# Kernel tuning notes

Hardware: AMD Instinct MI355X
Metric: run time of the kernel (lower is better)

Reference implementation:

```python
import jax, jax.numpy as jnp
import numpy as np

N = 16384      # nodes per graph (128x128 image)
E = 9 * N      # 8-neighborhood + self edges
C = 512        # input feature channels
M = 32         # matrixSize


def _p(key, shape, scale=0.05):
    return jax.random.normal(key, shape, dtype=jnp.float32) * scale


def setup_inputs() -> dict:
    key = jax.random.key(0)
    ks = jax.random.split(key, 40)
    inp = {
        "cF": jax.random.normal(ks[0], (N, C), dtype=jnp.float32),
        "sF": jax.random.normal(ks[1], (N, C), dtype=jnp.float32),
        "content_edge_index": jax.random.randint(ks[2], (2, E), 0, N),
        "content_selections": jax.random.randint(ks[3], (E,), 0, 9),
        "style_edge_index": jax.random.randint(ks[4], (2, E), 0, N),
        "style_selections": jax.random.randint(ks[5], (E,), 0, 9),
        "compress_W": _p(ks[6], (1, C, M)),   # kernel_size=1 -> 1 selection
        "compress_b": _p(ks[7], (M,)),
        "unzip_W": _p(ks[8], (1, M, C)),
        "unzip_b": _p(ks[9], (C,)),
    }
    i = 10
    for net in ("cnet", "snet"):
        for j, (ci, co) in enumerate([(C, 256), (256, 128), (128, M)], 1):
            inp[f"{net}_W{j}"] = _p(ks[i], (9, ci, co)); i += 1  # kernel_size=3 -> 9 selections
            inp[f"{net}_b{j}"] = _p(ks[i], (co,)); i += 1
        inp[f"{net}_fcW"] = _p(ks[i], (M * M, M * M)); i += 1   # torch Linear [out,in]
        inp[f"{net}_fcb"] = _p(ks[i], (M * M,)); i += 1
    return inp


def sel_conv(x, edge_index, sel, W, b):
    """SelectionConv: per-selection weight, gather from src, scatter-add to dst.
    x: [N,Cin], W: [S,Cin,Cout]. Edges with selection >= S are masked (kernel_size=1)."""
    S = W.shape[0]
    t = jnp.einsum('nc,scd->snd', x, W)              # [S, N, Cout]
    src, dst = edge_index[0], edge_index[1]
    msgs = t[jnp.minimum(sel, S - 1), src]           # [E, Cout]
    msgs = jnp.where((sel < S)[:, None], msgs, 0.0)
    return jax.ops.segment_sum(msgs, dst, num_segments=x.shape[0]) + b


def cnn_net(x, ei, sel, W1, b1, W2, b2, W3, b3, fcW, fcb):
    h = jax.nn.relu(sel_conv(x, ei, sel, W1, b1))
    h = jax.nn.relu(sel_conv(h, ei, sel, W2, b2))
    h = sel_conv(h, ei, sel, W3, b3)                 # [N, M]
    g = (h.T @ h) / h.shape[0]                       # [M, M] gram
    return g.reshape(-1) @ fcW.T + fcb               # [M*M]


def reference(cF, sF, content_edge_index, content_selections, style_edge_index,
              style_selections, compress_W, compress_b, unzip_W, unzip_b,
              cnet_W1, cnet_b1, cnet_W2, cnet_b2, cnet_W3, cnet_b3, cnet_fcW, cnet_fcb,
              snet_W1, snet_b1, snet_W2, snet_b2, snet_W3, snet_b3, snet_fcW, snet_fcb):
    cMean = jnp.mean(cF, axis=0, keepdims=True)
    cFc = cF - cMean
    sMean = jnp.mean(sF, axis=0, keepdims=True)
    sFc = sF - sMean
    compress_content = sel_conv(cFc, content_edge_index, content_selections,
                                compress_W, compress_b)          # [N, M]
    m = compress_W.shape[2]
    cMat = cnn_net(cFc, content_edge_index, content_selections,
                   cnet_W1, cnet_b1, cnet_W2, cnet_b2, cnet_W3, cnet_b3,
                   cnet_fcW, cnet_fcb).reshape(m, m)
    sMat = cnn_net(sFc, style_edge_index, style_selections,
                   snet_W1, snet_b1, snet_W2, snet_b2, snet_W3, snet_b3,
                   snet_fcW, snet_fcb).reshape(m, m)
    transmatrix = sMat @ cMat                                    # [M, M]
    transfeature = (transmatrix @ compress_content.T).T          # [N, M]
    out = sel_conv(transfeature, content_edge_index, content_selections,
                   unzip_W, unzip_b) + sMean                     # [N, 512]
    return (out, transmatrix)
```

## Files before the change

### kernel.cpp

```cpp
#include <hip/hip_runtime.h>
#include <hip/hip_bf16.h>
#include <cstddef>
#include <cstdint>

#define NN 16384
#define EE (9*NN)
#define CC 512

typedef __attribute__((ext_vector_type(4))) float f32x4;
typedef __attribute__((ext_vector_type(8))) short bf16x8;

static inline int idiv(int a, int b){ return (a+b-1)/b; }

__device__ __forceinline__ float bf2f(unsigned short u){
    union{unsigned u; float f;} v; v.u = ((unsigned)u) << 16; return v.f;
}
__device__ __forceinline__ unsigned short f2bf(float f){
    union{float f; unsigned u;} v; v.f = f;
    unsigned r = v.u + 0x7fffu + ((v.u >> 16) & 1u);
    return (unsigned short)(r >> 16);
}

__device__ __forceinline__ void gload16(const void* gsrc, void* ldst){
    __builtin_amdgcn_global_load_lds(
        (const __attribute__((address_space(1))) unsigned int*)gsrc,
        (__attribute__((address_space(3))) unsigned int*)ldst,
        16, 0, 0);
}


__global__ void zero_i(int* __restrict__ p, int n){
    int i = blockIdx.x*256 + threadIdx.x; if (i < n) p[i] = 0;
}

__global__ void colsum2(const float* __restrict__ F0, float* __restrict__ cs0,
                        const float* __restrict__ F1, float* __restrict__ cs1){
    const float* F = blockIdx.z ? F1 : F0;
    float* cs = blockIdx.z ? cs1 : cs0;
    const int RPB = NN/256;
    int r0 = blockIdx.x * RPB;
    int c4 = threadIdx.x;
    float4 s = {0.f,0.f,0.f,0.f};
    for (int r = 0; r < RPB; ++r){
        float4 v = ((const float4*)(F + (size_t)(r0+r)*CC))[c4];
        s.x += v.x; s.y += v.y; s.z += v.z; s.w += v.w;
    }
    atomicAdd(&cs[c4*4+0], s.x);
    atomicAdd(&cs[c4*4+1], s.y);
    atomicAdd(&cs[c4*4+2], s.z);
    atomicAdd(&cs[c4*4+3], s.w);
}

__global__ void center2(const float* __restrict__ F0, const float* __restrict__ cs0,
                        ushort4* __restrict__ o0,
                        const float* __restrict__ F1, const float* __restrict__ cs1,
                        ushort4* __restrict__ o1){
    const float* F = blockIdx.z ? F1 : F0;
    const float* cs = blockIdx.z ? cs1 : cs0;
    ushort4* o = blockIdx.z ? o1 : o0;
    int i = blockIdx.x*256 + threadIdx.x;
    float4 v = ((const float4*)F)[i];
    int c = (i << 2) & (CC-1);
    float4 m = *(const float4*)(cs + c);
    ushort4 r;
    r.x = f2bf(v.x - m.x*(1.f/NN));
    r.y = f2bf(v.y - m.y*(1.f/NN));
    r.z = f2bf(v.z - m.z*(1.f/NN));
    r.w = f2bf(v.w - m.w*(1.f/NN));
    o[i] = r;
}

__global__ void wtrans(const float* __restrict__ W, unsigned short* __restrict__ Wt,
                       int S, int K, int Cout, int Npad, int Kpad){
    int idx = blockIdx.x*256 + threadIdx.x;
    if (idx >= Npad*Kpad) return;
    int colp = idx / Kpad, k = idx - colp*Kpad;
    int s = colp / Cout, j = colp - s*Cout;
    float v = 0.f;
    if (s < S && k < K) v = W[((size_t)s*K + k)*Cout + j];
    Wt[idx] = f2bf(v);
}

__global__ void wtrans2z(const float* __restrict__ W0, const float* __restrict__ W1,
                         unsigned short* __restrict__ Wt0, unsigned short* __restrict__ Wt1,
                         int K, int Cout){
    __shared__ float tile[32][129];
    int s = blockIdx.z % 9;
    const float* W = (blockIdx.z < 9) ? W0 : W1;
    unsigned short* Wt = (blockIdx.z < 9) ? Wt0 : Wt1;
    int jb = blockIdx.x*128, kb = blockIdx.y*32;
    const float* Ws = W + (size_t)s*K*Cout;
    for (int r = 0; r < 32; ++r)
        tile[r][threadIdx.x] = Ws[(size_t)(kb+r)*Cout + jb + threadIdx.x];
    __syncthreads();
    int kk = threadIdx.x & 31, j0 = threadIdx.x >> 5;
    for (int jj = j0; jj < 128; jj += 4)
        Wt[(size_t)(s*Cout + jb + jj)*K + kb + kk] = f2bf(tile[kk][jj]);
}

__global__ void csr_count3(const int* __restrict__ cDst, const int* __restrict__ sDst,
                           const int* __restrict__ cSel,
                           int* __restrict__ cCnt, int* __restrict__ sCnt, int* __restrict__ cCnt0){
    int e = blockIdx.x*256 + threadIdx.x;
    if (e >= EE) return;
    int z = blockIdx.z;
    if (z == 0)      atomicAdd(&cCnt[cDst[e]], 1);
    else if (z == 1) atomicAdd(&sCnt[sDst[e]], 1);
    else if (cSel[e] == 0) atomicAdd(&cCnt0[cDst[e]], 1);
}
__global__ void csr_scan3(const int* __restrict__ c0, const int* __restrict__ c1,
                          const int* __restrict__ c2,
                          int* __restrict__ r0, int* __restrict__ r1, int* __restrict__ r2){
    const int* cnt = blockIdx.z==0 ? c0 : (blockIdx.z==1 ? c1 : c2);
    int* rowptr    = blockIdx.z==0 ? r0 : (blockIdx.z==1 ? r1 : r2);
    __shared__ int part[1024];
    int t = threadIdx.x;
    int base = t*16, s = 0;
    int local[16];
    #pragma unroll
    for (int i = 0; i < 16; ++i){ local[i] = s; s += cnt[base+i]; }
    part[t] = s; __syncthreads();
    for (int off = 1; off < 1024; off <<= 1){
        int v = (t >= off) ? part[t-off] : 0;
        __syncthreads();
        part[t] += v;
        __syncthreads();
    }
    int pre = (t == 0) ? 0 : part[t-1];
    #pragma unroll
    for (int i = 0; i < 16; ++i) rowptr[base+i] = pre + local[i];
    if (t == 1023) rowptr[NN] = part[1023];
}
__global__ void csr_fill3(const int* __restrict__ cSrc, const int* __restrict__ cDst,
                          const int* __restrict__ cSel,
                          const int* __restrict__ sSrc, const int* __restrict__ sDst,
                          const int* __restrict__ sSel,
                          const int* __restrict__ cRow, const int* __restrict__ sRow,
                          const int* __restrict__ cRow0,
                          int* __restrict__ cCur, int* __restrict__ sCur, int* __restrict__ cCur0,
                          int* __restrict__ cEl, int* __restrict__ sEl, int* __restrict__ cEl0){
    int e = blockIdx.x*256 + threadIdx.x;
    if (e >= EE) return;
    int z = blockIdx.z;
    if (z == 0){
        int d = cDst[e];
        int p = atomicAdd(&cCur[d], 1);
        cEl[cRow[d] + p] = (cSrc[e] << 4) | cSel[e];
    } else if (z == 1){
        int d = sDst[e];
        int p = atomicAdd(&sCur[d], 1);
        sEl[sRow[d] + p] = (sSrc[e] << 4) | sSel[e];
    } else if (cSel[e] == 0){
        int d = cDst[e];
        int p = atomicAdd(&cCur0[d], 1);
        cEl0[cRow0[d] + p] = cSrc[e];
    }
}

template<typename OutT>
__global__ __launch_bounds__(256, 2)
void mfma_gemm(const unsigned short* __restrict__ A0, const unsigned short* __restrict__ Bt0,
               OutT* __restrict__ C0,
               const unsigned short* __restrict__ A1, const unsigned short* __restrict__ Bt1,
               OutT* __restrict__ C1, int K, int N){
    const unsigned short* A  = blockIdx.z ? A1 : A0;
    const unsigned short* Bt = blockIdx.z ? Bt1 : Bt0;
    OutT* C = blockIdx.z ? C1 : C0;
    __shared__ __align__(16) unsigned short As[128*64];
    __shared__ __align__(16) unsigned short Bs[128*64];
    const int tid  = threadIdx.x;
    const int wave = tid >> 6, lane = tid & 63;
    const int row0 = blockIdx.y << 7, col0 = blockIdx.x << 7;
    const int wm = wave >> 1, wn = wave & 1;
    const int fr = lane & 15, fq = lane >> 4;
    f32x4 acc[4][4] = {};
    for (int k0 = 0; k0 < K; k0 += 64){
        __syncthreads();
        #pragma unroll
        for (int i = 0; i < 4; ++i){
            int chb = (wave*4 + i) * 64;
            int ch  = chb + lane;
            int r   = ch >> 3, c8 = ch & 7;
            gload16((const char*)(A  + (size_t)(row0 + r)*K + k0) + c8*16, As + chb*8);
            gload16((const char*)(Bt + (size_t)(col0 + r)*K + k0) + c8*16, Bs + chb*8);
        }
        __syncthreads();
        #pragma unroll
        for (int ks = 0; ks < 2; ++ks){
            bf16x8 av[4], bv[4];
            #pragma unroll
            for (int m = 0; m < 4; ++m)
                av[m] = *(const bf16x8*)(As + ((wm<<6)+(m<<4)+fr)*64 + (ks<<5) + (fq<<3));
            #pragma unroll
            for (int n = 0; n < 4; ++n)
                bv[n] = *(const bf16x8*)(Bs + ((wn<<6)+(n<<4)+fr)*64 + (ks<<5) + (fq<<3));
            #pragma unroll
            for (int m = 0; m < 4; ++m)
                #pragma unroll
                for (int n = 0; n < 4; ++n)
                    acc[m][n] = __builtin_amdgcn_mfma_f32_16x16x32_bf16(bv[n], av[m], acc[m][n], 0, 0, 0);
        }
    }
    #pragma unroll
    for (int m = 0; m < 4; ++m){
        int row = row0 + (wm<<6) + (m<<4) + fr;
        OutT* crow = C + (size_t)row*N + col0 + (wn<<6) + (fq<<2);
        #pragma unroll
        for (int n = 0; n < 4; ++n){
            if constexpr (sizeof(OutT) == 2){
                unsigned lo = f2bf(acc[m][n][0]) | ((unsigned)f2bf(acc[m][n][1]) << 16);
                unsigned hi = f2bf(acc[m][n][2]) | ((unsigned)f2bf(acc[m][n][3]) << 16);
                uint2 pk; pk.x = lo; pk.y = hi;
                *(uint2*)((unsigned short*)crow + (n<<4)) = pk;
            } else {
                float4 pk; pk.x = acc[m][n][0]; pk.y = acc[m][n][1];
                pk.z = acc[m][n][2]; pk.w = acc[m][n][3];
                *(float4*)((float*)crow + (n<<4)) = pk;
            }
        }
    }
}

template<int MQ, int NQ>
__device__ __forceinline__ void mfmaq(f32x4 (&acc)[8][4], bf16x8 (&a)[4][2], bf16x8 (&b)[2][2]){
    #pragma unroll
    for (int m = 0; m < 4; ++m)
        #pragma unroll
        for (int n = 0; n < 2; ++n)
            #pragma unroll
            for (int ks = 0; ks < 2; ++ks)
                acc[MQ*4+m][NQ*2+n] = __builtin_amdgcn_mfma_f32_16x16x32_bf16(
                    b[n][ks], a[m][ks], acc[MQ*4+m][NQ*2+n], 0, 0, 0);
}

#define MIDBAR() do{ __builtin_amdgcn_s_barrier(); \
                     asm volatile("s_waitcnt lgkmcnt(0)" ::: "memory"); \
                     __builtin_amdgcn_sched_barrier(0); \
                     __builtin_amdgcn_s_setprio(1); }while(0)
#define ENDBAR() do{ __builtin_amdgcn_s_setprio(0); \
                     __builtin_amdgcn_s_barrier(); }while(0)

template<int NK>
__global__ __launch_bounds__(512, 1)
void gemm8p(const unsigned short* __restrict__ Ain0, const unsigned short* __restrict__ Btin0,
            unsigned short* __restrict__ Cout0,
            const unsigned short* __restrict__ Ain1, const unsigned short* __restrict__ Btin1,
            unsigned short* __restrict__ Cout1, int N){
    constexpr int LDK = NK*64;
    const unsigned short* A  = blockIdx.z ? Ain1 : Ain0;
    const unsigned short* Bt = blockIdx.z ? Btin1 : Btin0;
    unsigned short* C = blockIdx.z ? Cout1 : Cout0;
    __shared__ __align__(16) unsigned short lds[2][4][8192];
    const int tid = threadIdx.x, w = tid >> 6, l = tid & 63;
    const int nbx = gridDim.x;
    const int nwg = gridDim.x * gridDim.y;
    int blin = blockIdx.y * nbx + blockIdx.x;
    int sw = (blin & 7) * (nwg >> 3) + (blin >> 3);
    const int bx = sw % nbx, by = sw / nbx;
    const int row0 = by << 8, col0 = bx << 8;
    const int wm = w >> 2, wn = w & 3;
    const int fr = l & 15, fq = l >> 4;

    f32x4 acc[8][4] = {};
    bf16x8 a[4][2], b01[2][2], b23[2][2];

    const unsigned short* gA = A + (size_t)row0 * LDK;
    const unsigned short* gB = Bt + (size_t)col0 * LDK;

    auto STG = [&](const unsigned short* gbase, int t, int half, unsigned short* ldsHalf){
        #pragma unroll
        for (int s = 0; s < 2; ++s){
            int o = s*8192 + w*1024 + l*16;
            int q = o ^ ((o >> 3) & 0x70);
            int row = q >> 7;
            gload16((const char*)(gbase + (size_t)(half*128 + row)*LDK + t*64) + (q & 127),
                    ldsHalf + s*4096 + w*512);
        }
    };
    auto LDA = [&](const unsigned short* half, int rb, int ks){
        int lg = (rb*16 + fr)*128 + ks*64 + fq*16;
        int ph = lg ^ ((fr & 7) << 4);
        return *(const bf16x8*)((const char*)half + ph);
    };

    STG(gA, 0, 0, &lds[0][0][0]); STG(gA, 0, 1, &lds[0][1][0]);
    STG(gB, 0, 0, &lds[0][2][0]); STG(gB, 0, 1, &lds[0][3][0]);
    STG(gB, 1, 0, &lds[1][2][0]); STG(gB, 1, 1, &lds[1][3][0]);
    asm volatile("s_waitcnt vmcnt(4)" ::: "memory");
    __builtin_amdgcn_s_barrier();

    const unsigned short* myA[2] = { &lds[0][wm][0], &lds[1][wm][0] };
    const unsigned short* myB[2] = { &lds[0][2+(wn>>1)][0], &lds[1][2+(wn>>1)][0] };
    const int brb = (wn & 1) * 4;

    for (int i = 0; i < NK/2; ++i){
        const int t0 = 2*i, t1 = 2*i + 1;
        #pragma unroll
        for (int m = 0; m < 4; ++m){ a[m][0] = LDA(myA[0], m, 0); a[m][1] = LDA(myA[0], m, 1); }
        #pragma unroll
        for (int n = 0; n < 2; ++n){ b01[n][0] = LDA(myB[0], brb+n, 0); b01[n][1] = LDA(myB[0], brb+n, 1); }
        STG(gA, t1, 0, &lds[1][0][0]);
        MIDBAR(); mfmaq<0,0>(acc, a, b01); ENDBAR();
        #pragma unroll
        for (int n = 0; n < 2; ++n){ b23[n][0] = LDA(myB[0], brb+2+n, 0); b23[n][1] = LDA(myB[0], brb+2+n, 1); }
        STG(gA, t1, 1, &lds[1][1][0]);
        MIDBAR(); mfmaq<0,1>(acc, a, b23); ENDBAR();
        #pragma unroll
        for (int m = 0; m < 4; ++m){ a[m][0] = LDA(myA[0], 4+m, 0); a[m][1] = LDA(myA[0], 4+m, 1); }
        STG(gB, t0+2, 0, &lds[0][2][0]);
        MIDBAR(); mfmaq<1,0>(acc, a, b01); ENDBAR();
        STG(gB, t0+2, 1, &lds[0][3][0]);
        asm volatile("s_waitcnt vmcnt(4)" ::: "memory");
        MIDBAR(); mfmaq<1,1>(acc, a, b23); ENDBAR();
        #pragma unroll
        for (int m = 0; m < 4; ++m){ a[m][0] = LDA(myA[1], m, 0); a[m][1] = LDA(myA[1], m, 1); }
        #pragma unroll
        for (int n = 0; n < 2; ++n){ b01[n][0] = LDA(myB[1], brb+n, 0); b01[n][1] = LDA(myB[1], brb+n, 1); }
        STG(gA, t0+2, 0, &lds[0][0][0]);
        MIDBAR(); mfmaq<0,0>(acc, a, b01); ENDBAR();
        #pragma unroll
        for (int n = 0; n < 2; ++n){ b23[n][0] = LDA(myB[1], brb+2+n, 0); b23[n][1] = LDA(myB[1], brb+2+n, 1); }
        STG(gA, t0+2, 1, &lds[0][1][0]);
        MIDBAR(); mfmaq<0,1>(acc, a, b23); ENDBAR();
        #pragma unroll
        for (int m = 0; m < 4; ++m){ a[m][0] = LDA(myA[1], 4+m, 0); a[m][1] = LDA(myA[1], 4+m, 1); }
        STG(gB, t1+2, 0, &lds[1][2][0]);
        MIDBAR(); mfmaq<1,0>(acc, a, b01); ENDBAR();
        STG(gB, t1+2, 1, &lds[1][3][0]);
        asm volatile("s_waitcnt vmcnt(4)" ::: "memory");
        MIDBAR(); mfmaq<1,1>(acc, a, b23); ENDBAR();
    }
    asm volatile("s_waitcnt vmcnt(0)" ::: "memory");

    #pragma unroll
    for (int m = 0; m < 8; ++m){
        int row = row0 + wm*128 + m*16 + fr;
        unsigned short* crow = C + (size_t)row*N + col0 + wn*64 + fq*4;
        #pragma unroll
        for (int n = 0; n < 4; ++n){
            unsigned lo = f2bf(acc[m][n][0]) | ((unsigned)f2bf(acc[m][n][1]) << 16);
            unsigned hi = f2bf(acc[m][n][2]) | ((unsigned)f2bf(acc[m][n][3]) << 16);
            uint2 pk; pk.x = lo; pk.y = hi;
            *(uint2*)(crow + (n<<4)) = pk;
        }
    }
}

template<typename TO, bool RELU>
__global__ void gather8z(const int* __restrict__ rp0, const int* __restrict__ el0,
                         const unsigned short* __restrict__ t0, const float* __restrict__ b0,
                         TO* __restrict__ o0,
                         const int* __restrict__ rp1, const int* __restrict__ el1,
                         const unsigned short* __restrict__ t1, const float* __restrict__ b1,
                         TO* __restrict__ o1,
                         int tStride, int coutShift){
    const int* rowptr = blockIdx.z ? rp1 : rp0;
    const int* elist  = blockIdx.z ? el1 : el0;
    const unsigned short* t = blockIdx.z ? t1 : t0;
    const float* bias = blockIdx.z ? b1 : b0;
    TO* out = blockIdx.z ? o1 : o0;
    int idx = blockIdx.x*256 + threadIdx.x;
    int chSh = coutShift - 3;
    int d = idx >> chSh;
    int c0 = (idx & ((1 << chSh) - 1)) << 3;
    float acc[8];
    {
        const float4* bb = (const float4*)(bias + c0);
        float4 a = bb[0], b = bb[1];
        acc[0]=a.x; acc[1]=a.y; acc[2]=a.z; acc[3]=a.w;
        acc[4]=b.x; acc[5]=b.y; acc[6]=b.z; acc[7]=b.w;
    }
    int j1 = rowptr[d+1];
    #pragma unroll 2
    for (int j = rowptr[d]; j < j1; ++j){
        int p = elist[j];
        int s = p & 15, sr = p >> 4;
        bf16x8 v = *(const bf16x8*)(t + (size_t)sr*tStride + (s << coutShift) + c0);
        #pragma unroll
        for (int k = 0; k < 8; ++k) acc[k] += bf2f((unsigned short)v[k]);
    }
    if (RELU){
        #pragma unroll
        for (int k = 0; k < 8; ++k) acc[k] = fmaxf(acc[k], 0.f);
    }
    if constexpr (sizeof(TO) == 2){
        union { bf16x8 v; unsigned short u[8]; } r;
        #pragma unroll
        for (int k = 0; k < 8; ++k) r.u[k] = f2bf(acc[k]);
        *(bf16x8*)((unsigned short*)out + ((size_t)d << coutShift) + c0) = r.v;
    } else {
        float4 a = {acc[0],acc[1],acc[2],acc[3]};
        float4 b = {acc[4],acc[5],acc[6],acc[7]};
        float4* op = (float4*)((float*)out + ((size_t)d << coutShift) + c0);
        op[0] = a; op[1] = b;
    }
}

template<bool ADDV>
__global__ void gather4f(const int* __restrict__ rowptr, const int* __restrict__ elist,
                         const float* __restrict__ t,
                         const float* __restrict__ bias, const float* __restrict__ addvec,
                         float* __restrict__ out, int tStride, int coutShift){
    int idx = blockIdx.x*256 + threadIdx.x;
    int chSh = coutShift - 2;
    int d = idx >> chSh;
    int c0 = (idx & ((1 << chSh) - 1)) << 2;
    float4 bb = *(const float4*)(bias + c0);
    float acc0 = bb.x, acc1 = bb.y, acc2 = bb.z, acc3 = bb.w;
    if (ADDV){
        float4 av = *(const float4*)(addvec + c0);
        acc0 += av.x*(1.f/NN); acc1 += av.y*(1.f/NN);
        acc2 += av.z*(1.f/NN); acc3 += av.w*(1.f/NN);
    }
    int j1 = rowptr[d+1];
    #pragma unroll 2
    for (int j = rowptr[d]; j < j1; ++j){
        int sr = elist[j];
        float4 v = *(const float4*)(t + (size_t)sr*tStride + c0);
        acc0 += v.x; acc1 += v.y; acc2 += v.z; acc3 += v.w;
    }
    float4 r = {acc0, acc1, acc2, acc3};
    *(float4*)(out + ((size_t)d << coutShift) + c0) = r;
}

__global__ void gram2(const float* __restrict__ h0, float* __restrict__ g0,
                      const float* __restrict__ h1, float* __restrict__ g1){
    const float* h = blockIdx.z ? h1 : h0;
    float* g = blockIdx.z ? g1 : g0;
    const int RPB = NN/64;
    int r0 = blockIdx.x*RPB;
    int i = threadIdx.x >> 5, j = threadIdx.x & 31;
    float s = 0.f;
    for (int r = 0; r < RPB; ++r){
        const float* row = h + (size_t)(r0+r)*32;
        s += row[i]*row[j];
    }
    atomicAdd(&g[threadIdx.x], s);
}

__global__ void fc2(const float* __restrict__ g0, const float* __restrict__ fcW0,
                    const float* __restrict__ fcb0, float* __restrict__ o0,
                    const float* __restrict__ g1, const float* __restrict__ fcW1,
                    const float* __restrict__ fcb1, float* __restrict__ o1){
    const float* g   = blockIdx.z ? g1 : g0;
    const float* fcW = blockIdx.z ? fcW1 : fcW0;
    const float* fcb = blockIdx.z ? fcb1 : fcb0;
    float* outMat    = blockIdx.z ? o1 : o0;
    int i = blockIdx.x;
    float s = 0.f;
    for (int j = threadIdx.x; j < 1024; j += 256)
        s += g[j] * (1.f/NN) * fcW[(size_t)i*1024 + j];
    __shared__ float red[256];
    red[threadIdx.x] = s; __syncthreads();
    for (int off = 128; off > 0; off >>= 1){
        if (threadIdx.x < off) red[threadIdx.x] += red[threadIdx.x+off];
        __syncthreads();
    }
    if (threadIdx.x == 0) outMat[i] = red[0] + fcb[i];
}

__global__ void mm32_kernel(const float* __restrict__ A, const float* __restrict__ B,
                            float* __restrict__ T){
    int i = threadIdx.x >> 5, j = threadIdx.x & 31;
    float s = 0.f;
    for (int k = 0; k < 32; ++k) s += A[i*32+k]*B[k*32+j];
    T[threadIdx.x] = s;
}

__global__ void tf_cvt_kernel(const float* __restrict__ cc, const float* __restrict__ T,
                              unsigned short* __restrict__ tfbB){
    __shared__ float Ts[1024];
    for (int i = threadIdx.x; i < 1024; i += blockDim.x) Ts[i] = T[i];
    __syncthreads();
    int idx = blockIdx.x*blockDim.x + threadIdx.x;
    int n = idx >> 5, i = idx & 31;
    float s = 0.f;
    const float* crow = cc + (size_t)n*32;
    #pragma unroll
    for (int j = 0; j < 32; ++j) s += crow[j] * Ts[i*32+j];
    tfbB[(size_t)n*64 + i] = f2bf(s);
    tfbB[(size_t)n*64 + 32 + i] = 0;
}

extern "C" void kernel_launch(void* const* d_in, const int* in_sizes, int n_in,
                              void* d_out, int out_size, void* d_ws, size_t ws_size,
                              hipStream_t stream){
    const float* cF   = (const float*)d_in[0];
    const float* sF   = (const float*)d_in[1];
    const int*   cEI  = (const int*)d_in[2];
    const int*   cSel = (const int*)d_in[3];
    const int*   sEI  = (const int*)d_in[4];
    const int*   sSel = (const int*)d_in[5];
    const float* compW= (const float*)d_in[6];
    const float* compB= (const float*)d_in[7];
    const float* unzW = (const float*)d_in[8];
    const float* unzB = (const float*)d_in[9];
    const float* cW1=(const float*)d_in[10]; const float* cB1=(const float*)d_in[11];
    const float* cW2=(const float*)d_in[12]; const float* cB2=(const float*)d_in[13];
    const float* cW3=(const float*)d_in[14]; const float* cB3=(const float*)d_in[15];
    const float* cFW=(const float*)d_in[16]; const float* cFB=(const float*)d_in[17];
    const float* sW1=(const float*)d_in[18]; const float* sB1=(const float*)d_in[19];
    const float* sW2=(const float*)d_in[20]; const float* sB2=(const float*)d_in[21];
    const float* sW3=(const float*)d_in[22]; const float* sB3=(const float*)d_in[23];
    const float* sFW=(const float*)d_in[24]; const float* sFB=(const float*)d_in[25];

    float* out  = (float*)d_out;
    float* Tmat = out + (size_t)NN*CC;

    char* w = (char*)d_ws;
    auto alloc = [&](size_t b)->char*{ char* p = w; w += (b + 255) & ~(size_t)255; return p; };
    float* cCol = (float*)alloc(512*4);
    float* sCol = (float*)alloc(512*4);
    float* cg   = (float*)alloc(1024*4);
    float* sg   = (float*)alloc(1024*4);
    float* cMat = (float*)alloc(1024*4);
    float* sMat = (float*)alloc(1024*4);
    int* cCnt = (int*)alloc(NN*4);
    int* cCur = (int*)alloc(NN*4);
    int* sCnt = (int*)alloc(NN*4);
    int* sCur = (int*)alloc(NN*4);
    int* cCnt0= (int*)alloc(NN*4);
    int* cCur0= (int*)alloc(NN*4);
    int* cRow = (int*)alloc((NN+1)*4);
    int* sRow = (int*)alloc((NN+1)*4);
    int* cRow0= (int*)alloc((NN+1)*4);
    int* cEl  = (int*)alloc(EE*4);
    int* sEl  = (int*)alloc(EE*4);
    int* cEl0 = (int*)alloc(EE*4);
    float* ccbuf = (float*)alloc((size_t)NN*32*4);
    unsigned short* tfbB = (unsigned short*)alloc((size_t)NN*64*2);
    unsigned short* wtC1 = (unsigned short*)alloc((size_t)2304*512*2);
    unsigned short* wtC2 = (unsigned short*)alloc((size_t)1280*256*2);
    unsigned short* wtC3 = (unsigned short*)alloc((size_t)384*128*2);
    unsigned short* wtS1 = (unsigned short*)alloc((size_t)2304*512*2);
    unsigned short* wtS2 = (unsigned short*)alloc((size_t)1280*256*2);
    unsigned short* wtS3 = (unsigned short*)alloc((size_t)384*128*2);
    unsigned short* wtCo = (unsigned short*)alloc((size_t)128*512*2);
    unsigned short* wtU  = (unsigned short*)alloc((size_t)512*64*2);
    unsigned short* cFcB = (unsigned short*)alloc((size_t)NN*512*2);
    unsigned short* sFcB = (unsigned short*)alloc((size_t)NN*512*2);
    float* h3c = (float*)alloc((size_t)NN*32*4);
    float* h3s = (float*)alloc((size_t)NN*32*4);
    unsigned short* tC = (unsigned short*)alloc((size_t)NN*2304*2);
    unsigned short* tS = (unsigned short*)alloc((size_t)NN*2304*2);
    float* tFc = (float*)tC;
    unsigned short* h1c = cFcB;
    unsigned short* h1s = sFcB;
    unsigned short* h2c = cFcB + (size_t)NN*256;
    unsigned short* h2s = sFcB + (size_t)NN*256;

    const int* cSrc = cEI; const int* cDst = cEI + EE;
    const int* sSrc = sEI; const int* sDst = sEI + EE;

    int zeroInts = (int)(((char*)cCur0 - (char*)d_ws)/4) + NN;
    zero_i<<<idiv(zeroInts,256),256,0,stream>>>((int*)d_ws, zeroInts);

    colsum2<<<dim3(256,1,2),128,0,stream>>>(cF, cCol, sF, sCol);
    center2<<<dim3(NN*CC/1024,1,2),256,0,stream>>>(cF, cCol, (ushort4*)cFcB,
                                                   sF, sCol, (ushort4*)sFcB);

    wtrans2z<<<dim3(2,16,18),128,0,stream>>>(cW1, sW1, wtC1, wtS1, 512, 256);
    wtrans2z<<<dim3(1,8,18),128,0,stream>>>(cW2, sW2, wtC2, wtS2, 256, 128);
    wtrans<<<idiv(384*128,256),256,0,stream>>>(cW3, wtC3, 9,128,32, 384,128);
    wtrans<<<idiv(384*128,256),256,0,stream>>>(sW3, wtS3, 9,128,32, 384,128);
    wtrans<<<idiv(128*512,256),256,0,stream>>>(compW, wtCo, 1,512,32, 128,512);
    wtrans<<<idiv(512*64,256),256,0,stream>>>(unzW,  wtU,  1,32,512, 512,64);

    csr_count3<<<dim3(idiv(EE,256),1,3),256,0,stream>>>(cDst, sDst, cSel, cCnt, sCnt, cCnt0);
    csr_scan3<<<dim3(1,1,3),1024,0,stream>>>(cCnt, sCnt, cCnt0, cRow, sRow, cRow0);
    csr_fill3<<<dim3(idiv(EE,256),1,3),256,0,stream>>>(cSrc,cDst,cSel, sSrc,sDst,sSel,
                                                       cRow,sRow,cRow0, cCur,sCur,cCur0,
                                                       cEl,sEl,cEl0);

    mfma_gemm<float><<<dim3(1,128,1),256,0,stream>>>(cFcB, wtCo, tFc, cFcB, wtCo, tFc, 512, 128);
    gather4f<false><<<NN*8/256,256,0,stream>>>(cRow0,cEl0,tFc,compB,nullptr,ccbuf,128,5);

    gemm8p<8><<<dim3(9,64,2),512,0,stream>>>(cFcB, wtC1, tC, sFcB, wtS1, tS, 2304);
    gather8z<unsigned short,true><<<dim3(2048,1,2),256,0,stream>>>(
        cRow,cEl,tC,cB1,h1c, sRow,sEl,tS,sB1,h1s, 2304, 8);
    gemm8p<4><<<dim3(5,64,2),512,0,stream>>>(h1c, wtC2, tC, h1s, wtS2, tS, 1280);
    gather8z<unsigned short,true><<<dim3(1024,1,2),256,0,stream>>>(
        cRow,cEl,tC,cB2,h2c, sRow,sEl,tS,sB2,h2s, 1280, 7);
    mfma_gemm<unsigned short><<<dim3(3,128,2),256,0,stream>>>(h2c, wtC3, tC, h2s, wtS3, tS, 128, 384);
    gather8z<float,false><<<dim3(256,1,2),256,0,stream>>>(
        cRow,cEl,tC,cB3,h3c, sRow,sEl,tS,sB3,h3s, 384, 5);
    gram2<<<dim3(64,1,2),1024,0,stream>>>(h3c, cg, h3s, sg);
    fc2<<<dim3(1024,1,2),256,0,stream>>>(cg,cFW,cFB,cMat, sg,sFW,sFB,sMat);

    mm32_kernel<<<1,1024,0,stream>>>(sMat, cMat, Tmat);
    tf_cvt_kernel<<<NN*32/256,256,0,stream>>>(ccbuf, Tmat, tfbB);

    mfma_gemm<float><<<dim3(4,128,1),256,0,stream>>>(tfbB, wtU, tFc, tfbB, wtU, tFc, 64, 512);
    gather4f<true><<<NN*128/256,256,0,stream>>>(cRow0,cEl0,tFc,unzB,sCol,out,512,9);
}
```

Measured before the change: 438.2 us.

## Fold mean-centering into GEMM epilogue and unify GEMMs into double-buffered kernel

Drops the separate centering pass. The raw features are converted to bf16 during the column-sum pass, and the mean is subtracted afterwards as a precomputed mean·W correction in the GEMM epilogue. All GEMMs, including the heavily hand-pipelined 256x256 gemm8p, are replaced by one 128x128 double-buffered kernel with a swizzled LDS layout and 3 blocks per CU. The small 32x32 matmul is fused into the transfeature conversion kernel, and several tiny weight-transposition launches are merged. Precision changes because the uncentered features are rounded to bf16, and dropping the tuned large-tile GEMM may cost throughput on the biggest layer.

```diff
diff --git a/kernel.cpp b/kernel.cpp
--- a/kernel.cpp
+++ b/kernel.cpp
@@ -33,10 +33,13 @@
     int i = blockIdx.x*256 + threadIdx.x; if (i < n) p[i] = 0;
 }
 
-__global__ void colsum2(const float* __restrict__ F0, float* __restrict__ cs0,
-                        const float* __restrict__ F1, float* __restrict__ cs1){
+__global__ void colsum_cvt(const float* __restrict__ F0, float* __restrict__ cs0,
+                           ushort4* __restrict__ o0,
+                           const float* __restrict__ F1, float* __restrict__ cs1,
+                           ushort4* __restrict__ o1){
     const float* F = blockIdx.z ? F1 : F0;
     float* cs = blockIdx.z ? cs1 : cs0;
+    ushort4* o = blockIdx.z ? o1 : o0;
     const int RPB = NN/256;
     int r0 = blockIdx.x * RPB;
     int c4 = threadIdx.x;
@@ -44,6 +47,9 @@
     for (int r = 0; r < RPB; ++r){
         float4 v = ((const float4*)(F + (size_t)(r0+r)*CC))[c4];
         s.x += v.x; s.y += v.y; s.z += v.z; s.w += v.w;
+        ushort4 u;
+        u.x = f2bf(v.x); u.y = f2bf(v.y); u.z = f2bf(v.z); u.w = f2bf(v.w);
+        o[(size_t)(r0+r)*(CC/4) + c4] = u;
     }
     atomicAdd(&cs[c4*4+0], s.x);
     atomicAdd(&cs[c4*4+1], s.y);
@@ -51,27 +57,29 @@
     atomicAdd(&cs[c4*4+3], s.w);
 }
 
-__global__ void center2(const float* __restrict__ F0, const float* __restrict__ cs0,
-                        ushort4* __restrict__ o0,
-                        const float* __restrict__ F1, const float* __restrict__ cs1,
-                        ushort4* __restrict__ o1){
-    const float* F = blockIdx.z ? F1 : F0;
+__global__ void mw_k(const float* __restrict__ W0, const float* __restrict__ cs0,
+                     float* __restrict__ mw0,
+                     const float* __restrict__ W1, const float* __restrict__ cs1,
+                     float* __restrict__ mw1,
+                     int S, int K, int Cout, int Npad){
+    const float* W = blockIdx.z ? W1 : W0;
     const float* cs = blockIdx.z ? cs1 : cs0;
-    ushort4* o = blockIdx.z ? o1 : o0;
-    int i = blockIdx.x*256 + threadIdx.x;
-    float4 v = ((const float4*)F)[i];
-    int c = (i << 2) & (CC-1);
-    float4 m = *(const float4*)(cs + c);
-    ushort4 r;
-    r.x = f2bf(v.x - m.x*(1.f/NN));
-    r.y = f2bf(v.y - m.y*(1.f/NN));
-    r.z = f2bf(v.z - m.z*(1.f/NN));
-    r.w = f2bf(v.w - m.w*(1.f/NN));
-    o[i] = r;
-}
-
-__global__ void wtrans(const float* __restrict__ W, unsigned short* __restrict__ Wt,
-                       int S, int K, int Cout, int Npad, int Kpad){
+    float* mw = blockIdx.z ? mw1 : mw0;
+    int colp = blockIdx.x*256 + threadIdx.x;
+    if (colp >= Npad) return;
+    int s = colp / Cout, j = colp - s*Cout;
+    float acc = 0.f;
+    if (s < S){
+        for (int c = 0; c < K; ++c) acc += cs[c] * W[((size_t)s*K + c)*Cout + j];
+    }
+    mw[colp] = acc * (1.f/NN);
+}
+
+__global__ void wtransz(const float* __restrict__ W0, unsigned short* __restrict__ Wt0,
+                        const float* __restrict__ W1, unsigned short* __restrict__ Wt1,
+                        int S, int K, int Cout, int Npad, int Kpad){
+    const float* W = blockIdx.z ? W1 : W0;
+    unsigned short* Wt = blockIdx.z ? Wt1 : Wt0;
     int idx = blockIdx.x*256 + threadIdx.x;
     if (idx >= Npad*Kpad) return;
     int colp = idx / Kpad, k = idx - colp*Kpad;
@@ -157,191 +165,93 @@
     }
 }
 
-template<typename OutT>
-__global__ __launch_bounds__(256, 2)
-void mfma_gemm(const unsigned short* __restrict__ A0, const unsigned short* __restrict__ Bt0,
-               OutT* __restrict__ C0,
-               const unsigned short* __restrict__ A1, const unsigned short* __restrict__ Bt1,
-               OutT* __restrict__ C1, int K, int N){
+template<int NT, typename OutT>
+__global__ __launch_bounds__(256, 3)
+void gemm_db(const unsigned short* __restrict__ A0, const unsigned short* __restrict__ Bt0,
+             OutT* __restrict__ C0, const float* __restrict__ csub0,
+             const unsigned short* __restrict__ A1, const unsigned short* __restrict__ Bt1,
+             OutT* __restrict__ C1, const float* __restrict__ csub1, int N){
+    constexpr int LDK = NT*32;
     const unsigned short* A  = blockIdx.z ? A1 : A0;
     const unsigned short* Bt = blockIdx.z ? Bt1 : Bt0;
     OutT* C = blockIdx.z ? C1 : C0;
-    __shared__ __align__(16) unsigned short As[128*64];
-    __shared__ __align__(16) unsigned short Bs[128*64];
-    const int tid  = threadIdx.x;
-    const int wave = tid >> 6, lane = tid & 63;
-    const int row0 = blockIdx.y << 7, col0 = blockIdx.x << 7;
-    const int wm = wave >> 1, wn = wave & 1;
-    const int fr = lane & 15, fq = lane >> 4;
-    f32x4 acc[4][4] = {};
-    for (int k0 = 0; k0 < K; k0 += 64){
-        __syncthreads();
-        #pragma unroll
-        for (int i = 0; i < 4; ++i){
-            int chb = (wave*4 + i) * 64;
-            int ch  = chb + lane;
-            int r   = ch >> 3, c8 = ch & 7;
-            gload16((const char*)(A  + (size_t)(row0 + r)*K + k0) + c8*16, As + chb*8);
-            gload16((const char*)(Bt + (size_t)(col0 + r)*K + k0) + c8*16, Bs + chb*8);
-        }
-        __syncthreads();
-        #pragma unroll
-        for (int ks = 0; ks < 2; ++ks){
-            bf16x8 av[4], bv[4];
-            #pragma unroll
-            for (int m = 0; m < 4; ++m)
-                av[m] = *(const bf16x8*)(As + ((wm<<6)+(m<<4)+fr)*64 + (ks<<5) + (fq<<3));
-            #pragma unroll
-            for (int n = 0; n < 4; ++n)
-                bv[n] = *(const bf16x8*)(Bs + ((wn<<6)+(n<<4)+fr)*64 + (ks<<5) + (fq<<3));
-            #pragma unroll
-            for (int m = 0; m < 4; ++m)
-                #pragma unroll
-                for (int n = 0; n < 4; ++n)
-                    acc[m][n] = __builtin_amdgcn_mfma_f32_16x16x32_bf16(bv[n], av[m], acc[m][n], 0, 0, 0);
-        }
-    }
-    #pragma unroll
-    for (int m = 0; m < 4; ++m){
-        int row = row0 + (wm<<6) + (m<<4) + fr;
-        OutT* crow = C + (size_t)row*N + col0 + (wn<<6) + (fq<<2);
-        #pragma unroll
-        for (int n = 0; n < 4; ++n){
-            if constexpr (sizeof(OutT) == 2){
-                unsigned lo = f2bf(acc[m][n][0]) | ((unsigned)f2bf(acc[m][n][1]) << 16);
-                unsigned hi = f2bf(acc[m][n][2]) | ((unsigned)f2bf(acc[m][n][3]) << 16);
-                uint2 pk; pk.x = lo; pk.y = hi;
-                *(uint2*)((unsigned short*)crow + (n<<4)) = pk;
-            } else {
-                float4 pk; pk.x = acc[m][n][0]; pk.y = acc[m][n][1];
-                pk.z = acc[m][n][2]; pk.w = acc[m][n][3];
-                *(float4*)((float*)crow + (n<<4)) = pk;
-            }
-        }
-    }
-}
-
-template<int MQ, int NQ>
-__device__ __forceinline__ void mfmaq(f32x4 (&acc)[8][4], bf16x8 (&a)[4][2], bf16x8 (&b)[2][2]){
-    #pragma unroll
-    for (int m = 0; m < 4; ++m)
-        #pragma unroll
-        for (int n = 0; n < 2; ++n)
-            #pragma unroll
-            for (int ks = 0; ks < 2; ++ks)
-                acc[MQ*4+m][NQ*2+n] = __builtin_amdgcn_mfma_f32_16x16x32_bf16(
-                    b[n][ks], a[m][ks], acc[MQ*4+m][NQ*2+n], 0, 0, 0);
-}
-
-#define MIDBAR() do{ __builtin_amdgcn_s_barrier(); \
-                     asm volatile("s_waitcnt lgkmcnt(0)" ::: "memory"); \
-                     __builtin_amdgcn_sched_barrier(0); \
-                     __builtin_amdgcn_s_setprio(1); }while(0)
-#define ENDBAR() do{ __builtin_amdgcn_s_setprio(0); \
-                     __builtin_amdgcn_s_barrier(); }while(0)
-
-template<int NK>
-__global__ __launch_bounds__(512, 1)
-void gemm8p(const unsigned short* __restrict__ Ain0, const unsigned short* __restrict__ Btin0,
-            unsigned short* __restrict__ Cout0,
-            const unsigned short* __restrict__ Ain1, const unsigned short* __restrict__ Btin1,
-            unsigned short* __restrict__ Cout1, int N){
-    constexpr int LDK = NK*64;
-    const unsigned short* A  = blockIdx.z ? Ain1 : Ain0;
-    const unsigned short* Bt = blockIdx.z ? Btin1 : Btin0;
-    unsigned short* C = blockIdx.z ? Cout1 : Cout0;
-    __shared__ __align__(16) unsigned short lds[2][4][8192];
+    const float* csub = blockIdx.z ? csub1 : csub0;
+    __shared__ __align__(16) unsigned short lds[2][2][4096];
     const int tid = threadIdx.x, w = tid >> 6, l = tid & 63;
+    const int wm = w >> 1, wn = w & 1;
+    const int fr = l & 15, fq = l >> 4;
     const int nbx = gridDim.x;
     const int nwg = gridDim.x * gridDim.y;
     int blin = blockIdx.y * nbx + blockIdx.x;
     int sw = (blin & 7) * (nwg >> 3) + (blin >> 3);
     const int bx = sw % nbx, by = sw / nbx;
-    const int row0 = by << 8, col0 = bx << 8;
-    const int wm = w >> 2, wn = w & 3;
-    const int fr = l & 15, fq = l >> 4;
-
-    f32x4 acc[8][4] = {};
-    bf16x8 a[4][2], b01[2][2], b23[2][2];
+    const int row0 = by << 7, col0 = bx << 7;
 
     const unsigned short* gA = A + (size_t)row0 * LDK;
     const unsigned short* gB = Bt + (size_t)col0 * LDK;
 
-    auto STG = [&](const unsigned short* gbase, int t, int half, unsigned short* ldsHalf){
-        #pragma unroll
-        for (int s = 0; s < 2; ++s){
-            int o = s*8192 + w*1024 + l*16;
-            int q = o ^ ((o >> 3) & 0x70);
-            int row = q >> 7;
-            gload16((const char*)(gbase + (size_t)(half*128 + row)*LDK + t*64) + (q & 127),
-                    ldsHalf + s*4096 + w*512);
+    auto STG = [&](int buf, int t){
+        #pragma unroll
+        for (int mtx = 0; mtx < 2; ++mtx){
+            const unsigned short* gb = mtx ? gB : gA;
+            #pragma unroll
+            for (int ld = 0; ld < 2; ++ld){
+                int o = (ld*256 + tid) * 16;
+                int row = o >> 6;
+                int kb = (o & 63) ^ ((row & 3) << 4);
+                gload16((const char*)(gb + (size_t)row*LDK + t*32) + kb,
+                        (char*)&lds[buf][mtx][0] + o);
+            }
         }
     };
-    auto LDA = [&](const unsigned short* half, int rb, int ks){
-        int lg = (rb*16 + fr)*128 + ks*64 + fq*16;
-        int ph = lg ^ ((fr & 7) << 4);
-        return *(const bf16x8*)((const char*)half + ph);
-    };
-
-    STG(gA, 0, 0, &lds[0][0][0]); STG(gA, 0, 1, &lds[0][1][0]);
-    STG(gB, 0, 0, &lds[0][2][0]); STG(gB, 0, 1, &lds[0][3][0]);
-    STG(gB, 1, 0, &lds[1][2][0]); STG(gB, 1, 1, &lds[1][3][0]);
-    asm volatile("s_waitcnt vmcnt(4)" ::: "memory");
-    __builtin_amdgcn_s_barrier();
-
-    const unsigned short* myA[2] = { &lds[0][wm][0], &lds[1][wm][0] };
-    const unsigned short* myB[2] = { &lds[0][2+(wn>>1)][0], &lds[1][2+(wn>>1)][0] };
-    const int brb = (wn & 1) * 4;
-
-    for (int i = 0; i < NK/2; ++i){
-        const int t0 = 2*i, t1 = 2*i + 1;
-        #pragma unroll
-        for (int m = 0; m < 4; ++m){ a[m][0] = LDA(myA[0], m, 0); a[m][1] = LDA(myA[0], m, 1); }
-        #pragma unroll
-        for (int n = 0; n < 2; ++n){ b01[n][0] = LDA(myB[0], brb+n, 0); b01[n][1] = LDA(myB[0], brb+n, 1); }
-        STG(gA, t1, 0, &lds[1][0][0]);
-        MIDBAR(); mfmaq<0,0>(acc, a, b01); ENDBAR();
-        #pragma unroll
-        for (int n = 0; n < 2; ++n){ b23[n][0] = LDA(myB[0], brb+2+n, 0); b23[n][1] = LDA(myB[0], brb+2+n, 1); }
-        STG(gA, t1, 1, &lds[1][1][0]);
-        MIDBAR(); mfmaq<0,1>(acc, a, b23); ENDBAR();
-        #pragma unroll
-        for (int m = 0; m < 4; ++m){ a[m][0] = LDA(myA[0], 4+m, 0); a[m][1] = LDA(myA[0], 4+m, 1); }
-        STG(gB, t0+2, 0, &lds[0][2][0]);
-        MIDBAR(); mfmaq<1,0>(acc, a, b01); ENDBAR();
-        STG(gB, t0+2, 1, &lds[0][3][0]);
-        asm volatile("s_waitcnt vmcnt(4)" ::: "memory");
-        MIDBAR(); mfmaq<1,1>(acc, a, b23); ENDBAR();
-        #pragma unroll
-        for (int m = 0; m < 4; ++m){ a[m][0] = LDA(myA[1], m, 0); a[m][1] = LDA(myA[1], m, 1); }
-        #pragma unroll
-        for (int n = 0; n < 2; ++n){ b01[n][0] = LDA(myB[1], brb+n, 0); b01[n][1] = LDA(myB[1], brb+n, 1); }
-        STG(gA, t0+2, 0, &lds[0][0][0]);
-        MIDBAR(); mfmaq<0,0>(acc, a, b01); ENDBAR();
-        #pragma unroll
-        for (int n = 0; n < 2; ++n){ b23[n][0] = LDA(myB[1], brb+2+n, 0); b23[n][1] = LDA(myB[1], brb+2+n, 1); }
-        STG(gA, t0+2, 1, &lds[0][1][0]);
-        MIDBAR(); mfmaq<0,1>(acc, a, b23); ENDBAR();
-        #pragma unroll
-        for (int m = 0; m < 4; ++m){ a[m][0] = LDA(myA[1], 4+m, 0); a[m][1] = LDA(myA[1], 4+m, 1); }
-        STG(gB, t1+2, 0, &lds[1][2][0]);
-        MIDBAR(); mfmaq<1,0>(acc, a, b01); ENDBAR();
-        STG(gB, t1+2, 1, &lds[1][3][0]);
-        asm volatile("s_waitcnt vmcnt(4)" ::: "memory");
-        MIDBAR(); mfmaq<1,1>(acc, a, b23); ENDBAR();
-    }
-    asm volatile("s_waitcnt vmcnt(0)" ::: "memory");
+
+    f32x4 acc[4][4] = {};
+    STG(0, 0);
+    __syncthreads();
+    for (int t = 0; t < NT; ++t){
+        int cur = t & 1;
+        if (t + 1 < NT) STG(cur ^ 1, t + 1);
+        bf16x8 av[4], bv[4];
+        #pragma unroll
+        for (int m = 0; m < 4; ++m){
+            int r = wm*64 + m*16 + fr;
+            int p = (r*64 + fq*16) ^ ((r & 3) << 4);
+            av[m] = *(const bf16x8*)((const char*)&lds[cur][0][0] + p);
+        }
+        #pragma unroll
+        for (int n = 0; n < 4; ++n){
+            int r = wn*64 + n*16 + fr;
+            int p = (r*64 + fq*16) ^ ((r & 3) << 4);
+            bv[n] = *(const bf16x8*)((const char*)&lds[cur][1][0] + p);
+        }
+        #pragma unroll
+        for (int m = 0; m < 4; ++m)
+            #pragma unroll
+            for (int n = 0; n < 4; ++n)
+                acc[m][n] = __builtin_amdgcn_mfma_f32_16x16x32_bf16(bv[n], av[m], acc[m][n], 0, 0, 0);
+        __syncthreads();
+    }
 
     #pragma unroll
-    for (int m = 0; m < 8; ++m){
-        int row = row0 + wm*128 + m*16 + fr;
-        unsigned short* crow = C + (size_t)row*N + col0 + wn*64 + fq*4;
+    for (int m = 0; m < 4; ++m){
+        int row = row0 + wm*64 + m*16 + fr;
+        OutT* crow = C + (size_t)row*N + col0 + (wn<<6) + (fq<<2);
         #pragma unroll
         for (int n = 0; n < 4; ++n){
-            unsigned lo = f2bf(acc[m][n][0]) | ((unsigned)f2bf(acc[m][n][1]) << 16);
-            unsigned hi = f2bf(acc[m][n][2]) | ((unsigned)f2bf(acc[m][n][3]) << 16);
-            uint2 pk; pk.x = lo; pk.y = hi;
-            *(uint2*)(crow + (n<<4)) = pk;
+            float v0 = acc[m][n][0], v1 = acc[m][n][1], v2 = acc[m][n][2], v3 = acc[m][n][3];
+            if (csub){
+                float4 sub = *(const float4*)(csub + col0 + (wn<<6) + (fq<<2) + (n<<4));
+                v0 -= sub.x; v1 -= sub.y; v2 -= sub.z; v3 -= sub.w;
+            }
+            if constexpr (sizeof(OutT) == 2){
+                unsigned lo = f2bf(v0) | ((unsigned)f2bf(v1) << 16);
+                unsigned hi = f2bf(v2) | ((unsigned)f2bf(v3) << 16);
+                uint2 pk; pk.x = lo; pk.y = hi;
+                *(uint2*)((unsigned short*)crow + (n<<4)) = pk;
+            } else {
+                float4 pk; pk.x = v0; pk.y = v1; pk.z = v2; pk.w = v3;
+                *(float4*)((float*)crow + (n<<4)) = pk;
+            }
         }
     }
 }
@@ -459,20 +369,20 @@
     if (threadIdx.x == 0) outMat[i] = red[0] + fcb[i];
 }
 
-__global__ void mm32_kernel(const float* __restrict__ A, const float* __restrict__ B,
-                            float* __restrict__ T){
-    int i = threadIdx.x >> 5, j = threadIdx.x & 31;
-    float s = 0.f;
-    for (int k = 0; k < 32; ++k) s += A[i*32+k]*B[k*32+j];
-    T[threadIdx.x] = s;
-}
-
-__global__ void tf_cvt_kernel(const float* __restrict__ cc, const float* __restrict__ T,
-                              unsigned short* __restrict__ tfbB){
+__global__ void tf_cvt2(const float* __restrict__ cc, const float* __restrict__ sM,
+                        const float* __restrict__ cM, float* __restrict__ Tout,
+                        unsigned short* __restrict__ tfbB){
     __shared__ float Ts[1024];
-    for (int i = threadIdx.x; i < 1024; i += blockDim.x) Ts[i] = T[i];
+    for (int e = threadIdx.x; e < 1024; e += 256){
+        int i = e >> 5, j = e & 31;
+        float s = 0.f;
+        #pragma unroll
+        for (int k = 0; k < 32; ++k) s += sM[i*32+k]*cM[k*32+j];
+        Ts[e] = s;
+        if (blockIdx.x == 0) Tout[e] = s;
+    }
     __syncthreads();
-    int idx = blockIdx.x*blockDim.x + threadIdx.x;
+    int idx = blockIdx.x*256 + threadIdx.x;
     int n = idx >> 5, i = idx & 31;
     float s = 0.f;
     const float* crow = cc + (size_t)n*32;
@@ -529,6 +439,9 @@
     int* cEl0 = (int*)alloc(EE*4);
     float* ccbuf = (float*)alloc((size_t)NN*32*4);
     unsigned short* tfbB = (unsigned short*)alloc((size_t)NN*64*2);
+    float* mwC1 = (float*)alloc(2304*4);
+    float* mwS1 = (float*)alloc(2304*4);
+    float* mwCo = (float*)alloc(128*4);
     unsigned short* wtC1 = (unsigned short*)alloc((size_t)2304*512*2);
     unsigned short* wtC2 = (unsigned short*)alloc((size_t)1280*256*2);
     unsigned short* wtC3 = (unsigned short*)alloc((size_t)384*128*2);
@@ -537,17 +450,17 @@
     unsigned short* wtS3 = (unsigned short*)alloc((size_t)384*128*2);
     unsigned short* wtCo = (unsigned short*)alloc((size_t)128*512*2);
     unsigned short* wtU  = (unsigned short*)alloc((size_t)512*64*2);
-    unsigned short* cFcB = (unsigned short*)alloc((size_t)NN*512*2);
-    unsigned short* sFcB = (unsigned short*)alloc((size_t)NN*512*2);
+    unsigned short* xBc = (unsigned short*)alloc((size_t)NN*512*2);
+    unsigned short* xBs = (unsigned short*)alloc((size_t)NN*512*2);
     float* h3c = (float*)alloc((size_t)NN*32*4);
     float* h3s = (float*)alloc((size_t)NN*32*4);
     unsigned short* tC = (unsigned short*)alloc((size_t)NN*2304*2);
     unsigned short* tS = (unsigned short*)alloc((size_t)NN*2304*2);
     float* tFc = (float*)tC;
-    unsigned short* h1c = cFcB;
-    unsigned short* h1s = sFcB;
-    unsigned short* h2c = cFcB + (size_t)NN*256;
-    unsigned short* h2s = sFcB + (size_t)NN*256;
+    unsigned short* h1c = xBc;
+    unsigned short* h1s = xBs;
+    unsigned short* h2c = xBc + (size_t)NN*256;
+    unsigned short* h2s = xBs + (size_t)NN*256;
 
     const int* cSrc = cEI; const int* cDst = cEI + EE;
     const int* sSrc = sEI; const int* sDst = sEI + EE;
@@ -555,16 +468,17 @@
     int zeroInts = (int)(((char*)cCur0 - (char*)d_ws)/4) + NN;
     zero_i<<<idiv(zeroInts,256),256,0,stream>>>((int*)d_ws, zeroInts);
 
-    colsum2<<<dim3(256,1,2),128,0,stream>>>(cF, cCol, sF, sCol);
-    center2<<<dim3(NN*CC/1024,1,2),256,0,stream>>>(cF, cCol, (ushort4*)cFcB,
-                                                   sF, sCol, (ushort4*)sFcB);
+    colsum_cvt<<<dim3(256,1,2),128,0,stream>>>(cF, cCol, (ushort4*)xBc,
+                                               sF, sCol, (ushort4*)xBs);
 
     wtrans2z<<<dim3(2,16,18),128,0,stream>>>(cW1, sW1, wtC1, wtS1, 512, 256);
     wtrans2z<<<dim3(1,8,18),128,0,stream>>>(cW2, sW2, wtC2, wtS2, 256, 128);
-    wtrans<<<idiv(384*128,256),256,0,stream>>>(cW3, wtC3, 9,128,32, 384,128);
-    wtrans<<<idiv(384*128,256),256,0,stream>>>(sW3, wtS3, 9,128,32, 384,128);
-    wtrans<<<idiv(128*512,256),256,0,stream>>>(compW, wtCo, 1,512,32, 128,512);
-    wtrans<<<idiv(512*64,256),256,0,stream>>>(unzW,  wtU,  1,32,512, 512,64);
+    wtransz<<<dim3(idiv(384*128,256),1,2),256,0,stream>>>(cW3, wtC3, sW3, wtS3, 9,128,32, 384,128);
+    wtransz<<<dim3(idiv(128*512,256),1,1),256,0,stream>>>(compW, wtCo, compW, wtCo, 1,512,32, 128,512);
+    wtransz<<<dim3(idiv(512*64,256),1,1),256,0,stream>>>(unzW, wtU, unzW, wtU, 1,32,512, 512,64);
+
+    mw_k<<<dim3(9,1,2),256,0,stream>>>(cW1, cCol, mwC1, sW1, sCol, mwS1, 9,512,256, 2304);
+    mw_k<<<dim3(1,1,1),256,0,stream>>>(compW, cCol, mwCo, compW, cCol, mwCo, 1,512,32, 128);
 
     csr_count3<<<dim3(idiv(EE,256),1,3),256,0,stream>>>(cDst, sDst, cSel, cCnt, sCnt, cCnt0);
     csr_scan3<<<dim3(1,1,3),1024,0,stream>>>(cCnt, sCnt, cCnt0, cRow, sRow, cRow0);
@@ -572,24 +486,28 @@
                                                        cRow,sRow,cRow0, cCur,sCur,cCur0,
                                                        cEl,sEl,cEl0);
 
-    mfma_gemm<float><<<dim3(1,128,1),256,0,stream>>>(cFcB, wtCo, tFc, cFcB, wtCo, tFc, 512, 128);
+    gemm_db<16,float><<<dim3(1,128,1),256,0,stream>>>(xBc, wtCo, tFc, mwCo,
+                                                      xBc, wtCo, tFc, mwCo, 128);
     gather4f<false><<<NN*8/256,256,0,stream>>>(cRow0,cEl0,tFc,compB,nullptr,ccbuf,128,5);
 
-    gemm8p<8><<<dim3(9,64,2),512,0,stream>>>(cFcB, wtC1, tC, sFcB, wtS1, tS, 2304);
+    gemm_db<16,unsigned short><<<dim3(18,128,2),256,0,stream>>>(xBc, wtC1, tC, mwC1,
+                                                                xBs, wtS1, tS, mwS1, 2304);
     gather8z<unsigned short,true><<<dim3(2048,1,2),256,0,stream>>>(
         cRow,cEl,tC,cB1,h1c, sRow,sEl,tS,sB1,h1s, 2304, 8);
-    gemm8p<4><<<dim3(5,64,2),512,0,stream>>>(h1c, wtC2, tC, h1s, wtS2, tS, 1280);
+    gemm_db<8,unsigned short><<<dim3(10,128,2),256,0,stream>>>(h1c, wtC2, tC, nullptr,
+                                                               h1s, wtS2, tS, nullptr, 1280);
     gather8z<unsigned short,true><<<dim3(1024,1,2),256,0,stream>>>(
         cRow,cEl,tC,cB2,h2c, sRow,sEl,tS,sB2,h2s, 1280, 7);
-    mfma_gemm<unsigned short><<<dim3(3,128,2),256,0,stream>>>(h2c, wtC3, tC, h2s, wtS3, tS, 128, 384);
+    gemm_db<4,unsigned short><<<dim3(3,128,2),256,0,stream>>>(h2c, wtC3, tC, nullptr,
+                                                              h2s, wtS3, tS, nullptr, 384);
     gather8z<float,false><<<dim3(256,1,2),256,0,stream>>>(
         cRow,cEl,tC,cB3,h3c, sRow,sEl,tS,sB3,h3s, 384, 5);
     gram2<<<dim3(64,1,2),1024,0,stream>>>(h3c, cg, h3s, sg);
     fc2<<<dim3(1024,1,2),256,0,stream>>>(cg,cFW,cFB,cMat, sg,sFW,sFB,sMat);
 
-    mm32_kernel<<<1,1024,0,stream>>>(sMat, cMat, Tmat);
-    tf_cvt_kernel<<<NN*32/256,256,0,stream>>>(ccbuf, Tmat, tfbB);
-
-    mfma_gemm<float><<<dim3(4,128,1),256,0,stream>>>(tfbB, wtU, tFc, tfbB, wtU, tFc, 64, 512);
+    tf_cvt2<<<NN*32/256,256,0,stream>>>(ccbuf, sMat, cMat, Tmat, tfbB);
+
+    gemm_db<2,float><<<dim3(4,128,1),256,0,stream>>>(tfbB, wtU, tFc, nullptr,
+                                                     tfbB, wtU, tFc, nullptr, 512);
     gather4f<true><<<NN*128/256,256,0,stream>>>(cRow0,cEl0,tFc,unzB,sCol,out,512,9);
 }
```

Measured after the change: 610.2 us. +39.3%, slower.
